# Performance work log

Hardware: AMD Instinct MI355X
Metric: run time of the kernel (lower is better)

## Reference

```python
import jax, jax.numpy as jnp
import numpy as np


def setup_inputs() -> dict:
    key = jax.random.key(0)
    kq, kk, kv, km = jax.random.split(key, 4)
    B, H, S, D = 2, 16, 2048, 64
    Q = jax.random.normal(kq, (B, H, S, D), dtype=jnp.float32)
    K = jax.random.normal(kk, (B, H, S, D), dtype=jnp.float32)
    V = jax.random.normal(kv, (B, H, S, D), dtype=jnp.float32)
    attn_mask = jax.random.randint(km, (B, 1, S, S), 0, 2, dtype=jnp.int32)
    return {"Q": Q, "K": K, "V": V, "attn_mask": attn_mask}


def reference(Q, K, V, attn_mask):
    d_k = jnp.asarray(K.shape[-1], dtype=Q.dtype)
    # scores: [B,H,S,S]
    scores = jnp.einsum("bhqd,bhkd->bhqk", Q, K) / jnp.sqrt(d_k)
    scores = jnp.where(attn_mask == 0, jnp.asarray(-1e9, scores.dtype), scores)
    attn_weights = jax.nn.softmax(scores, axis=-1)
    context = jnp.einsum("bhqk,bhkd->bhqd", attn_weights, V)
    return context, attn_weights
```

## Files before the change

### kernel.cpp

```cpp
#include <hip/hip_runtime.h>
#include <hip/hip_bf16.h>

typedef __attribute__((ext_vector_type(8))) short      short8;
typedef __attribute__((ext_vector_type(4))) float      floatx4;
typedef unsigned long long u64;
typedef unsigned short     u16;

#define DI __device__ __forceinline__

constexpr int BB = 2, HH = 16, SS = 2048, DD = 64;
constexpr int TK  = 64;
constexpr int NKT = SS / TK;
constexpr int PB  = 72;

constexpr size_t NELEM  = (size_t)BB * HH * SS * DD;
constexpr size_t OFF_VT = NELEM * 2;
constexpr size_t OFF_MB = OFF_VT + NELEM * 2;

DI u16 f2bfu(float f) {
    __hip_bfloat16 h = __float2bfloat16(f);
    return __builtin_bit_cast(u16, h);
}

DI short8 pack8(floatx4 a, floatx4 b) {
    short8 r;
    r[0] = (short)f2bfu(a[0]); r[1] = (short)f2bfu(a[1]);
    r[2] = (short)f2bfu(a[2]); r[3] = (short)f2bfu(a[3]);
    r[4] = (short)f2bfu(b[0]); r[5] = (short)f2bfu(b[1]);
    r[6] = (short)f2bfu(b[2]); r[7] = (short)f2bfu(b[3]);
    return r;
}

DI short8 cvt8s(const float* __restrict__ p, float s) {
    floatx4 a = *(const floatx4*)p;
    floatx4 b = *(const floatx4*)(p + 4);
    a *= s; b *= s;
    return pack8(a, b);
}

constexpr int KBLK = 2048;
constexpr int VBLK = 1024;
constexpr int MBLK = 4096;

__global__ __launch_bounds__(256)
void prep_kernel(const float* __restrict__ K, const float* __restrict__ V,
                 const int* __restrict__ mask,
                 u16* __restrict__ Kb, u16* __restrict__ Vt, u64* __restrict__ Mb)
{
    const int bx = (int)blockIdx.x, tid = (int)threadIdx.x;
    if (bx < KBLK) {
        size_t i = ((size_t)bx * 256 + tid) * 8;
        floatx4 a = *(const floatx4*)(K + i);
        floatx4 b = *(const floatx4*)(K + i + 4);
        *(short8*)(Kb + i) = pack8(a, b);
    } else if (bx < KBLK + VBLK) {
        __shared__ __align__(16) u16 T[DD * 72];
        const int idx = bx - KBLK;
        const int bh = idx >> 5, kt = idx & 31;
        const int kvr = tid >> 2, d0 = (tid & 3) * 16;
        const float* vp = V + ((size_t)bh * SS + kt * 64 + kvr) * DD + d0;
        floatx4 v0 = *(const floatx4*)vp;
        floatx4 v1 = *(const floatx4*)(vp + 4);
        floatx4 v2 = *(const floatx4*)(vp + 8);
        floatx4 v3 = *(const floatx4*)(vp + 12);
#pragma unroll
        for (int i = 0; i < 4; ++i) T[(d0 + i)      * 72 + kvr] = f2bfu(v0[i]);
#pragma unroll
        for (int i = 0; i < 4; ++i) T[(d0 + 4 + i)  * 72 + kvr] = f2bfu(v1[i]);
#pragma unroll
        for (int i = 0; i < 4; ++i) T[(d0 + 8 + i)  * 72 + kvr] = f2bfu(v2[i]);
#pragma unroll
        for (int i = 0; i < 4; ++i) T[(d0 + 12 + i) * 72 + kvr] = f2bfu(v3[i]);
        __syncthreads();
        const int d = tid >> 2, seg = (tid & 3) * 16;
        short8 s0 = *(const short8*)&T[d * 72 + seg];
        short8 s1 = *(const short8*)&T[d * 72 + seg + 8];
        u16* op = Vt + ((size_t)bh * DD + d) * SS + kt * 64 + seg;
        *(short8*)op       = s0;
        *(short8*)(op + 8) = s1;
    } else {
        const int mc = bx - (KBLK + VBLK);
        const int wv = tid >> 6, lane = tid & 63;
        const size_t gw = (size_t)mc * 4 + wv;
#pragma unroll
        for (int it = 0; it < 8; ++it) {
            size_t word = gw * 8 + it;
            int b   = (int)(word >> 16);
            int rem = (int)(word & 65535);
            int q = rem >> 5, wj = rem & 31;
            int v = mask[((size_t)b * SS + q) * SS + wj * 64 + lane];
            u64 bal = __ballot(v != 0);
            if (lane == 0) Mb[word] = bal;
        }
    }
}

__global__ __launch_bounds__(64, 4)
void sdpa_main(const float* __restrict__ Q,
               const u16*   __restrict__ Kb,
               const u16*   __restrict__ Vt,
               const u64*   __restrict__ Mb,
               float*       __restrict__ out_ctx,
               float*       __restrict__ out_w)
{
    __shared__ __align__(16) u16 Pb[2 * 16 * PB];

    const int lane = (int)threadIdx.x;
    const int quad = lane >> 4;
    const int col  = lane & 15;

    const int id  = (int)blockIdx.x;
    const int nid = (id & 7) * 512 + (id >> 3);
    const int bh  = nid >> 7;
    const int q0  = (nid & 127) * 16;
    const int b   = bh >> 4;

    const size_t head = (size_t)bh * SS * DD;
    const u16* Kh = Kb + head;
    const u16* Vh = Vt + head;
    const u64* Mh = Mb + ((size_t)b * SS + q0) * (SS / 64);
    float*     Wh = out_w + (size_t)bh * SS * SS;

    short8 aQ0, aQ1;
    {
        const float* qp = Q + head + (size_t)(q0 + col) * DD + quad * 8;
        aQ0 = cvt8s(qp, 0.125f);
        aQ1 = cvt8s(qp + 32, 0.125f);
    }

    short8 kA[4], kB[4];
#pragma unroll
    for (int nt = 0; nt < 4; ++nt) {
        const u16* kp = Kh + (size_t)(nt * 16 + col) * DD + quad * 8;
        kA[nt] = *(const short8*)kp;
        kB[nt] = *(const short8*)(kp + 32);
    }

    float mrow[4], lrow[4];
#pragma unroll
    for (int r = 0; r < 4; ++r) { mrow[r] = -__builtin_inff(); lrow[r] = 0.f; }

    for (int kt = 0; kt < NKT; ++kt) {
        u64 mw[4];
#pragma unroll
        for (int r = 0; r < 4; ++r) mw[r] = Mh[(size_t)(quad * 4 + r) * (SS / 64) + kt];

        floatx4 acc[4];
        __builtin_amdgcn_s_setprio(1);
#pragma unroll
        for (int nt = 0; nt < 4; ++nt) {
            floatx4 a = {0.f, 0.f, 0.f, 0.f};
            a = __builtin_amdgcn_mfma_f32_16x16x32_bf16(aQ0, kA[nt], a, 0, 0, 0);
            a = __builtin_amdgcn_mfma_f32_16x16x32_bf16(aQ1, kB[nt], a, 0, 0, 0);
            acc[nt] = a;
        }
        __builtin_amdgcn_s_setprio(0);

        const int ktn = (kt + 1) & (NKT - 1);
#pragma unroll
        for (int nt = 0; nt < 4; ++nt) {
            const u16* kp = Kh + (size_t)(ktn * TK + nt * 16 + col) * DD + quad * 8;
            kA[nt] = *(const short8*)kp;
            kB[nt] = *(const short8*)(kp + 32);
        }

#pragma unroll
        for (int r = 0; r < 4; ++r) {
            float s[4];
#pragma unroll
            for (int nt = 0; nt < 4; ++nt) {
                unsigned mnt = (unsigned)(mw[r] >> (nt * 16));
                s[nt] = ((mnt >> col) & 1u) ? acc[nt][r] : -1e9f;
            }
            float lm = fmaxf(fmaxf(s[0], s[1]), fmaxf(s[2], s[3]));
            float mn = fmaxf(mrow[r], lm);
            float p  = __expf(s[0] - mn) + __expf(s[1] - mn) + __expf(s[2] - mn) + __expf(s[3] - mn);
            lrow[r]  = lrow[r] * __expf(mrow[r] - mn) + p;
            mrow[r]  = mn;
        }
    }
#pragma unroll
    for (int r = 0; r < 4; ++r) {
#pragma unroll
        for (int off = 1; off < 16; off <<= 1) {
            float mo = __shfl_xor(mrow[r], off);
            float lo = __shfl_xor(lrow[r], off);
            float mn = fmaxf(mrow[r], mo);
            lrow[r] = lrow[r] * __expf(mrow[r] - mn) + lo * __expf(mo - mn);
            mrow[r] = mn;
        }
    }
    float rl[4];
#pragma unroll
    for (int r = 0; r < 4; ++r) rl[r] = 1.0f / lrow[r];

    floatx4 ctx[4];
#pragma unroll
    for (int nt = 0; nt < 4; ++nt) ctx[nt] = floatx4{0.f, 0.f, 0.f, 0.f};

    for (int kt = 0; kt < NKT; ++kt) {
        const int kv0 = kt * TK;
        u16* Pl = &Pb[(kt & 1) * (16 * PB)];

        u64 mw[4];
#pragma unroll
        for (int r = 0; r < 4; ++r) mw[r] = Mh[(size_t)(quad * 4 + r) * (SS / 64) + kt];

        const int ktn = (kt + 1) & (NKT - 1);
        short8 vA[4], vB[4];

#pragma unroll
        for (int nt = 0; nt < 4; ++nt) {
            floatx4 a = {0.f, 0.f, 0.f, 0.f};
            __builtin_amdgcn_s_setprio(1);
            a = __builtin_amdgcn_mfma_f32_16x16x32_bf16(aQ0, kA[nt], a, 0, 0, 0);
            a = __builtin_amdgcn_mfma_f32_16x16x32_bf16(aQ1, kB[nt], a, 0, 0, 0);
            __builtin_amdgcn_s_setprio(0);

            {
                const u16* kp = Kh + (size_t)(ktn * TK + nt * 16 + col) * DD + quad * 8;
                kA[nt] = *(const short8*)kp;
                kB[nt] = *(const short8*)(kp + 32);
            }
            {
                const u16* vp = Vh + (size_t)(nt * 16 + col) * SS + kv0 + quad * 8;
                vA[nt] = *(const short8*)vp;
                vB[nt] = *(const short8*)(vp + 32);
            }

#pragma unroll
            for (int r = 0; r < 4; ++r) {
                const int rloc = quad * 4 + r;
                unsigned mnt = (unsigned)(mw[r] >> (nt * 16));
                float sv = ((mnt >> col) & 1u) ? a[r] : -1e9f;
                float w  = __expf(sv - mrow[r]) * rl[r];
                __builtin_nontemporal_store(w,
                    Wh + (size_t)(q0 + rloc) * SS + kv0 + nt * 16 + col);
                Pl[rloc * PB + nt * 16 + col] = f2bfu(w);
            }
        }

        asm volatile("s_waitcnt lgkmcnt(0)" ::: "memory");
        __builtin_amdgcn_sched_barrier(0);

        short8 pA0 = *(const short8*)&Pl[col * PB + quad * 8];
        short8 pA1 = *(const short8*)&Pl[col * PB + 32 + quad * 8];

        __builtin_amdgcn_s_setprio(1);
#pragma unroll
        for (int nt = 0; nt < 4; ++nt) {
            ctx[nt] = __builtin_amdgcn_mfma_f32_16x16x32_bf16(pA0, vA[nt], ctx[nt], 0, 0, 0);
            ctx[nt] = __builtin_amdgcn_mfma_f32_16x16x32_bf16(pA1, vB[nt], ctx[nt], 0, 0, 0);
        }
        __builtin_amdgcn_s_setprio(0);
    }

#pragma unroll
    for (int nt = 0; nt < 4; ++nt) {
#pragma unroll
        for (int r = 0; r < 4; ++r) {
            const int q = q0 + quad * 4 + r;
            __builtin_nontemporal_store(ctx[nt][r],
                out_ctx + head + (size_t)q * DD + nt * 16 + col);
        }
    }
}

extern "C" void kernel_launch(void* const* d_in, const int* in_sizes, int n_in,
                              void* d_out, int out_size, void* d_ws, size_t ws_size,
                              hipStream_t stream) {
    const float* Q = (const float*)d_in[0];
    const float* K = (const float*)d_in[1];
    const float* V = (const float*)d_in[2];
    const int* mask = (const int*)d_in[3];

    float* out     = (float*)d_out;
    float* out_ctx = out;
    float* out_w   = out + (size_t)BB * HH * SS * DD;

    u16* Kb = (u16*)d_ws;
    u16* Vt = (u16*)((char*)d_ws + OFF_VT);
    u64* Mb = (u64*)((char*)d_ws + OFF_MB);
    (void)ws_size;

    hipLaunchKernelGGL(prep_kernel, dim3(KBLK + VBLK + MBLK), dim3(256), 0, stream,
                       K, V, mask, Kb, Vt, Mb);
    hipLaunchKernelGGL(sdpa_main, dim3(SS / 16 * BB * HH), dim3(64), 0, stream,
                       Q, Kb, Vt, Mb, out_ctx, out_w);
}
```

Before: 964.8 us.

## Stage fp32 weights in LDS for vectorized stores, use two-wave blocks

The weight matrix is now written to a per-wave fp32 LDS tile and then streamed to global memory as 16-byte row-contiguous nontemporal stores, replacing scattered 4-byte stores. The bf16 P operand is then packed from that same LDS tile. Blocks now hold two waves covering 32 query rows, launched with a different occupancy hint. K and V register prefetching for the next tile is removed, and tiles are loaded just in time. This should improve store coalescing for the dominant weight output, but exposes more load latency and uses more LDS.

```diff
diff --git a/kernel.cpp b/kernel.cpp
--- a/kernel.cpp
+++ b/kernel.cpp
@@ -11,7 +11,7 @@
 constexpr int BB = 2, HH = 16, SS = 2048, DD = 64;
 constexpr int TK  = 64;
 constexpr int NKT = SS / TK;
-constexpr int PB  = 72;
+constexpr int PW  = 68;
 
 constexpr size_t NELEM  = (size_t)BB * HH * SS * DD;
 constexpr size_t OFF_VT = NELEM * 2;
@@ -95,7 +95,7 @@
     }
 }
 
-__global__ __launch_bounds__(64, 4)
+__global__ __launch_bounds__(128, 6)
 void sdpa_main(const float* __restrict__ Q,
                const u16*   __restrict__ Kb,
                const u16*   __restrict__ Vt,
@@ -103,16 +103,19 @@
                float*       __restrict__ out_ctx,
                float*       __restrict__ out_w)
 {
-    __shared__ __align__(16) u16 Pb[2 * 16 * PB];
-
-    const int lane = (int)threadIdx.x;
+    __shared__ __align__(16) float Pw[2][16 * PW];
+
+    const int tid  = (int)threadIdx.x;
+    const int wave = tid >> 6;
+    const int lane = tid & 63;
     const int quad = lane >> 4;
     const int col  = lane & 15;
+    float* Pl = Pw[wave];
 
     const int id  = (int)blockIdx.x;
-    const int nid = (id & 7) * 512 + (id >> 3);
-    const int bh  = nid >> 7;
-    const int q0  = (nid & 127) * 16;
+    const int nid = (id & 7) * 256 + (id >> 3);
+    const int bh  = nid >> 6;
+    const int q0  = (nid & 63) * 32 + wave * 16;
     const int b   = bh >> 4;
 
     const size_t head = (size_t)bh * SS * DD;
@@ -128,23 +131,23 @@
         aQ1 = cvt8s(qp + 32, 0.125f);
     }
 
-    short8 kA[4], kB[4];
-#pragma unroll
-    for (int nt = 0; nt < 4; ++nt) {
-        const u16* kp = Kh + (size_t)(nt * 16 + col) * DD + quad * 8;
-        kA[nt] = *(const short8*)kp;
-        kB[nt] = *(const short8*)(kp + 32);
-    }
-
     float mrow[4], lrow[4];
 #pragma unroll
     for (int r = 0; r < 4; ++r) { mrow[r] = -__builtin_inff(); lrow[r] = 0.f; }
 
     for (int kt = 0; kt < NKT; ++kt) {
+        const int kv0 = kt * TK;
         u64 mw[4];
 #pragma unroll
         for (int r = 0; r < 4; ++r) mw[r] = Mh[(size_t)(quad * 4 + r) * (SS / 64) + kt];
 
+        short8 kA[4], kB[4];
+#pragma unroll
+        for (int nt = 0; nt < 4; ++nt) {
+            const u16* kp = Kh + (size_t)(kv0 + nt * 16 + col) * DD + quad * 8;
+            kA[nt] = *(const short8*)kp;
+            kB[nt] = *(const short8*)(kp + 32);
+        }
         floatx4 acc[4];
         __builtin_amdgcn_s_setprio(1);
 #pragma unroll
@@ -155,14 +158,6 @@
             acc[nt] = a;
         }
         __builtin_amdgcn_s_setprio(0);
-
-        const int ktn = (kt + 1) & (NKT - 1);
-#pragma unroll
-        for (int nt = 0; nt < 4; ++nt) {
-            const u16* kp = Kh + (size_t)(ktn * TK + nt * 16 + col) * DD + quad * 8;
-            kA[nt] = *(const short8*)kp;
-            kB[nt] = *(const short8*)(kp + 32);
-        }
 
 #pragma unroll
         for (int r = 0; r < 4; ++r) {
@@ -200,51 +195,65 @@
 
     for (int kt = 0; kt < NKT; ++kt) {
         const int kv0 = kt * TK;
-        u16* Pl = &Pb[(kt & 1) * (16 * PB)];
 
         u64 mw[4];
 #pragma unroll
         for (int r = 0; r < 4; ++r) mw[r] = Mh[(size_t)(quad * 4 + r) * (SS / 64) + kt];
 
-        const int ktn = (kt + 1) & (NKT - 1);
-        short8 vA[4], vB[4];
-
+        short8 kA[4], kB[4];
+#pragma unroll
+        for (int nt = 0; nt < 4; ++nt) {
+            const u16* kp = Kh + (size_t)(kv0 + nt * 16 + col) * DD + quad * 8;
+            kA[nt] = *(const short8*)kp;
+            kB[nt] = *(const short8*)(kp + 32);
+        }
+        floatx4 acc[4];
+        __builtin_amdgcn_s_setprio(1);
 #pragma unroll
         for (int nt = 0; nt < 4; ++nt) {
             floatx4 a = {0.f, 0.f, 0.f, 0.f};
-            __builtin_amdgcn_s_setprio(1);
             a = __builtin_amdgcn_mfma_f32_16x16x32_bf16(aQ0, kA[nt], a, 0, 0, 0);
             a = __builtin_amdgcn_mfma_f32_16x16x32_bf16(aQ1, kB[nt], a, 0, 0, 0);
-            __builtin_amdgcn_s_setprio(0);
-
-            {
-                const u16* kp = Kh + (size_t)(ktn * TK + nt * 16 + col) * DD + quad * 8;
-                kA[nt] = *(const short8*)kp;
-                kB[nt] = *(const short8*)(kp + 32);
+            acc[nt] = a;
+        }
+        __builtin_amdgcn_s_setprio(0);
+
+#pragma unroll
+        for (int r = 0; r < 4; ++r) {
+            const int rloc = quad * 4 + r;
+#pragma unroll
+            for (int nt = 0; nt < 4; ++nt) {
+                unsigned mnt = (unsigned)(mw[r] >> (nt * 16));
+                float sv = ((mnt >> col) & 1u) ? acc[nt][r] : -1e9f;
+                Pl[rloc * PW + nt * 16 + col] = __expf(sv - mrow[r]) * rl[r];
             }
-            {
-                const u16* vp = Vh + (size_t)(nt * 16 + col) * SS + kv0 + quad * 8;
-                vA[nt] = *(const short8*)vp;
-                vB[nt] = *(const short8*)(vp + 32);
-            }
-
-#pragma unroll
-            for (int r = 0; r < 4; ++r) {
-                const int rloc = quad * 4 + r;
-                unsigned mnt = (unsigned)(mw[r] >> (nt * 16));
-                float sv = ((mnt >> col) & 1u) ? a[r] : -1e9f;
-                float w  = __expf(sv - mrow[r]) * rl[r];
-                __builtin_nontemporal_store(w,
-                    Wh + (size_t)(q0 + rloc) * SS + kv0 + nt * 16 + col);
-                Pl[rloc * PB + nt * 16 + col] = f2bfu(w);
-            }
+        }
+
+        short8 vA[4], vB[4];
+#pragma unroll
+        for (int nt = 0; nt < 4; ++nt) {
+            const u16* vp = Vh + (size_t)(nt * 16 + col) * SS + kv0 + quad * 8;
+            vA[nt] = *(const short8*)vp;
+            vB[nt] = *(const short8*)(vp + 32);
         }
 
         asm volatile("s_waitcnt lgkmcnt(0)" ::: "memory");
         __builtin_amdgcn_sched_barrier(0);
 
-        short8 pA0 = *(const short8*)&Pl[col * PB + quad * 8];
-        short8 pA1 = *(const short8*)&Pl[col * PB + 32 + quad * 8];
+#pragma unroll
+        for (int i = 0; i < 4; ++i) {
+            const int wr = quad + i * 4;
+            const int c4 = col * 4;
+            floatx4 wv = *(const floatx4*)&Pl[wr * PW + c4];
+            __builtin_nontemporal_store(wv, (floatx4*)(Wh + (size_t)(q0 + wr) * SS + kv0 + c4));
+        }
+
+        floatx4 pf0 = *(const floatx4*)&Pl[col * PW + quad * 8];
+        floatx4 pf1 = *(const floatx4*)&Pl[col * PW + quad * 8 + 4];
+        floatx4 pf2 = *(const floatx4*)&Pl[col * PW + 32 + quad * 8];
+        floatx4 pf3 = *(const floatx4*)&Pl[col * PW + 32 + quad * 8 + 4];
+        short8 pA0 = pack8(pf0, pf1);
+        short8 pA1 = pack8(pf2, pf3);
 
         __builtin_amdgcn_s_setprio(1);
 #pragma unroll
@@ -285,6 +294,6 @@
 
     hipLaunchKernelGGL(prep_kernel, dim3(KBLK + VBLK + MBLK), dim3(256), 0, stream,
                        K, V, mask, Kb, Vt, Mb);
-    hipLaunchKernelGGL(sdpa_main, dim3(SS / 16 * BB * HH), dim3(64), 0, stream,
+    hipLaunchKernelGGL(sdpa_main, dim3((SS / 32) * BB * HH), dim3(128), 0, stream,
                        Q, Kb, Vt, Mb, out_ctx, out_w);
 }
```

After: 974.7 us. About the same (+1.0%).
